# Kernel tuning notes

Hardware: AMD Instinct MI355X
Metric: run time of the kernel (lower is better)

Reference implementation:

```python
import jax, jax.numpy as jnp
import numpy as np
import math

N, C, H, W = 4, 256, 64, 64
CH = C // 2  # theta/phi output channels


def setup_inputs() -> dict:
    key = jax.random.key(0)
    k1, k2, k3 = jax.random.split(key, 3)
    x = jax.random.normal(k1, (N, C, H, W), dtype=jnp.float32)
    # 1x1 conv weights, init normal(0, 0.01) as in reset_params
    theta_w = 0.01 * jax.random.normal(k2, (CH, C), dtype=jnp.float32)
    phi_w = 0.01 * jax.random.normal(k3, (CH, C), dtype=jnp.float32)
    theta_b = jnp.zeros((CH,), dtype=jnp.float32)
    phi_b = jnp.zeros((CH,), dtype=jnp.float32)
    return {"x": x, "theta_w": theta_w, "theta_b": theta_b, "phi_w": phi_w, "phi_b": phi_b}


def reference(x, theta_w, theta_b, phi_w, phi_b):
    n, c, h, w = x.shape
    hw = h * w
    scale = 1.0 / math.sqrt(c)  # divide by sqrt(self.in_ch)
    # 1x1 convs (pointwise channel mixes)
    q = jnp.einsum('nchw,dc->ndhw', x, theta_w) + theta_b[None, :, None, None]
    k = jnp.einsum('nchw,dc->ndhw', x, phi_w) + phi_b[None, :, None, None]
    # affinity: [n, hw, hw] (flattened 'nabcd' tensor)
    q2 = q.reshape(n, c // 2, hw)
    k2 = k.reshape(n, c // 2, hw)
    ff = jnp.einsum('nis,nit->nst', q2, k2) * scale
    attn = jax.nn.softmax(ff, axis=-1)
    # weighted sum of values x: out[n,i,s] = sum_t attn[n,s,t] x[n,i,t]
    out = jnp.einsum('nst,nit->nis', attn, x.reshape(n, c, hw))
    return out.reshape(x.shape)
```

## Files before the change

### kernel.cpp

```cpp
#include <hip/hip_runtime.h>

#define S_LEN 4096
#define C_CH  256
#define D_CH  128
#define LAMBDA 0.09016844005555896f

typedef __attribute__((ext_vector_type(8)))  short short8;
typedef __attribute__((ext_vector_type(4)))  float f32x4;
typedef __attribute__((ext_vector_type(16))) float f32x16;

union PFrag { unsigned u[4]; short8 v; };

static __device__ __forceinline__ unsigned short f2bf(float x) {
    union { float f; unsigned u; } v; v.f = x;
    unsigned r = v.u + 0x7FFFu + ((v.u >> 16) & 1u);
    return (unsigned short)(r >> 16);
}

static __device__ __forceinline__ void gload_lds16(const void* g, void* l) {
    __builtin_amdgcn_global_load_lds(
        (const __attribute__((address_space(1))) void*)g,
        (__attribute__((address_space(3))) void*)l, 16, 0, 0);
}

__global__ void nlm_conv_kernel(const float* __restrict__ x, unsigned short* __restrict__ xb) {
    size_t base = ((size_t)blockIdx.x * 256 + threadIdx.x) * 4;
    float4 v = *reinterpret_cast<const float4*>(x + base);
    ushort4 b; b.x = f2bf(v.x); b.y = f2bf(v.y); b.z = f2bf(v.z); b.w = f2bf(v.w);
    *reinterpret_cast<ushort4*>(xb + base) = b;
}

__global__ void nlm_wconv_kernel(const float* __restrict__ tw, const float* __restrict__ pw,
                                 unsigned short* __restrict__ wb) {
    int base = (blockIdx.x * 256 + threadIdx.x) * 4;
    const float* src = (base < 32768) ? (tw + base) : (pw + base - 32768);
    float4 v = *reinterpret_cast<const float4*>(src);
    ushort4 b; b.x = f2bf(v.x); b.y = f2bf(v.y); b.z = f2bf(v.z); b.w = f2bf(v.w);
    *reinterpret_cast<ushort4*>(wb + base) = b;
}

__launch_bounds__(256, 1)
__global__ void nlm_proj_kernel(const float* __restrict__ x,
                                const unsigned short* __restrict__ wb,
                                const float* __restrict__ tb, const float* __restrict__ pbias,
                                unsigned char* __restrict__ Qb8, unsigned char* __restrict__ Kb8) {
    const int n    = blockIdx.y;
    const int wave = threadIdx.x >> 6;
    const int lane = threadIdx.x & 63;
    const int sl   = lane & 15, g = lane >> 4;
    const int s0   = blockIdx.x * 64 + wave * 16;
    const float* xn = x + (size_t)n * C_CH * S_LEN;

    f32x4 acc[16];
    #pragma unroll
    for (int i = 0; i < 16; ++i) acc[i] = (f32x4){0.f, 0.f, 0.f, 0.f};

    #pragma unroll 1
    for (int cc = 0; cc < 8; ++cc) {
        short8 af;
        #pragma unroll
        for (int j = 0; j < 8; ++j) {
            float v = xn[(size_t)(cc * 32 + g * 8 + j) * S_LEN + s0 + sl];
            af[j] = (short)f2bf(v);
        }
        #pragma unroll
        for (int t = 0; t < 16; ++t) {
            const unsigned short* wp = wb + (size_t)(t >> 3) * (D_CH * C_CH)
                                          + (size_t)((t & 7) * 16 + sl) * C_CH + cc * 32 + g * 8;
            short8 bf = *reinterpret_cast<const short8*>(wp);
            acc[t] = __builtin_amdgcn_mfma_f32_16x16x32_bf16(af, bf, acc[t], 0, 0, 0);
        }
    }
    #pragma unroll
    for (int t = 0; t < 16; ++t) {
        const float bias = (t < 8 ? tb : pbias)[(t & 7) * 16 + sl];
        unsigned char* dst = (t < 8 ? Qb8 : Kb8) + (size_t)n * S_LEN * D_CH;
        const int col = (t & 7) * 16 + sl;
        float v0 = acc[t][0] + bias, v1 = acc[t][1] + bias;
        float v2 = acc[t][2] + bias, v3 = acc[t][3] + bias;
        unsigned u01, u23;
        asm("v_cvt_pk_fp8_f32 %0, %1, %2" : "=v"(u01) : "v"(v0), "v"(v1));
        asm("v_cvt_pk_fp8_f32 %0, %1, %2" : "=v"(u23) : "v"(v2), "v"(v3));
        dst[(size_t)(s0 + g * 4 + 0) * D_CH + col] = (unsigned char)(u01 & 0xff);
        dst[(size_t)(s0 + g * 4 + 1) * D_CH + col] = (unsigned char)((u01 >> 8) & 0xff);
        dst[(size_t)(s0 + g * 4 + 2) * D_CH + col] = (unsigned char)(u23 & 0xff);
        dst[(size_t)(s0 + g * 4 + 3) * D_CH + col] = (unsigned char)((u23 >> 8) & 0xff);
    }
}

template<int TSPLIT>
__launch_bounds__(512, 2)
__global__ void nlm_attn_kernel(const unsigned char* __restrict__ Qb8,
                                const unsigned char* __restrict__ Kb8,
                                const unsigned short* __restrict__ xb,
                                float* __restrict__ part0, float* __restrict__ part1,
                                float* __restrict__ part2, float* __restrict__ part3,
                                float* __restrict__ lbuf) {
    constexpr int TRANGE = S_LEN / TSPLIT;
    constexpr int NITv   = TRANGE / 64;
    constexpr int TOTAL  = 64 * TSPLIT;
    const int sid  = blockIdx.x;
    const int newb = (sid & 7) * (TOTAL / 8) + (sid >> 3);
    const int n    = newb / (16 * TSPLIT);
    const int th   = (newb >> 4) & (TSPLIT - 1);
    const int sb   = newb & 15;
    const int lane = threadIdx.x & 63;
    const int wave = threadIdx.x >> 6;
    const int l31  = lane & 31;
    const int h    = lane >> 5;
    const int s0   = sb * 256 + wave * 32;
    const int tbase = th * TRANGE;

    __shared__ unsigned char  Klds[2][64 * 128];
    __shared__ unsigned short Vlds[2][256 * 64];

    const unsigned char* Qn8 = Qb8 + (size_t)n * S_LEN * D_CH;
    const unsigned char* Kn8 = Kb8 + (size_t)n * S_LEN * D_CH;
    const unsigned short* xn = xb + (size_t)n * C_CH * S_LEN;

    long qf8[8];
    #pragma unroll
    for (int ks = 0; ks < 8; ++ks)
        qf8[ks] = *reinterpret_cast<const long*>(Qn8 + (size_t)(s0 + l31) * D_CH + ks * 16 + h * 8);

    f32x16 oacc[8];
    #pragma unroll
    for (int i = 0; i < 8; ++i)
        #pragma unroll
        for (int r = 0; r < 16; ++r) oacc[i][r] = 0.f;
    float lsum = 0.f;

    auto kstage = [&](int itv, int slot) {
        const int it = itv < NITv ? itv : NITv - 1;
        const int t0 = tbase + it * 64;
        const int rl = wave * 8 + (lane >> 3);
        const int ch = (lane & 7) ^ (rl & 7);
        gload_lds16(Kn8 + (size_t)(t0 + rl) * D_CH + ch * 16,
                    &Klds[slot][wave * 8 * 128]);
    };
    auto vstage = [&](int itv, int slot) {
        const int it = itv < NITv ? itv : NITv - 1;
        const int t0 = tbase + it * 64;
        #pragma unroll
        for (int i = 0; i < 4; ++i) {
            const int row = wave * 32 + i * 8 + (lane >> 3);
            const int ch = (lane & 7) ^ (row & 7);
            gload_lds16(xn + (size_t)row * S_LEN + t0 + ch * 8,
                        &Vlds[slot][(wave * 32 + i * 8) * 64]);
        }
    };

    kstage(0, 0); vstage(0, 0);
    asm volatile("s_waitcnt vmcnt(0)" ::: "memory");

    #pragma unroll 1
    for (int it = 0; it < NITv; ++it) {
        const int cur = it & 1;
        __builtin_amdgcn_s_barrier();
        __builtin_amdgcn_sched_barrier(0);
        kstage(it + 1, cur ^ 1);
        vstage(it + 1, cur ^ 1);

        f32x16 sa, sb2;
        #pragma unroll
        for (int r = 0; r < 16; ++r) { sa[r] = 0.f; sb2[r] = 0.f; }
        const int f = l31 & 7;
        __builtin_amdgcn_s_setprio(1);
        #pragma unroll
        for (int ks = 0; ks < 8; ++ks) {
            const int co = ((ks ^ f) * 16) + h * 8;
            long kflo = *reinterpret_cast<const long*>(&Klds[cur][l31 * 128 + co]);
            long kfhi = *reinterpret_cast<const long*>(&Klds[cur][(32 + l31) * 128 + co]);
            sa  = __builtin_amdgcn_mfma_f32_32x32x16_fp8_fp8(kflo, qf8[ks], sa,  0, 0, 0);
            sb2 = __builtin_amdgcn_mfma_f32_32x32x16_fp8_fp8(kfhi, qf8[ks], sb2, 0, 0, 0);
        }
        __builtin_amdgcn_s_setprio(0);

        PFrag pa0, pa1, pa2, pa3;
        float rs = 0.f;
        {
            float p[16];
            #pragma unroll
            for (int r = 0; r < 16; ++r) { p[r] = __builtin_amdgcn_exp2f(sa[r] * LAMBDA); rs += p[r]; }
            unsigned W0, W1, W2, W3, W4, W5, W6, W7;
            asm("v_cvt_pk_bf16_f32 %0, %1, %2" : "=v"(W0) : "v"(p[0]),  "v"(p[1]));
            asm("v_cvt_pk_bf16_f32 %0, %1, %2" : "=v"(W1) : "v"(p[2]),  "v"(p[3]));
            asm("v_cvt_pk_bf16_f32 %0, %1, %2" : "=v"(W2) : "v"(p[4]),  "v"(p[5]));
            asm("v_cvt_pk_bf16_f32 %0, %1, %2" : "=v"(W3) : "v"(p[6]),  "v"(p[7]));
            asm("v_cvt_pk_bf16_f32 %0, %1, %2" : "=v"(W4) : "v"(p[8]),  "v"(p[9]));
            asm("v_cvt_pk_bf16_f32 %0, %1, %2" : "=v"(W5) : "v"(p[10]), "v"(p[11]));
            asm("v_cvt_pk_bf16_f32 %0, %1, %2" : "=v"(W6) : "v"(p[12]), "v"(p[13]));
            asm("v_cvt_pk_bf16_f32 %0, %1, %2" : "=v"(W7) : "v"(p[14]), "v"(p[15]));
            asm("v_permlane32_swap_b32 %0, %1" : "+v"(W0), "+v"(W2));
            asm("v_permlane32_swap_b32 %0, %1" : "+v"(W1), "+v"(W3));
            asm("v_permlane32_swap_b32 %0, %1" : "+v"(W4), "+v"(W6));
            asm("v_permlane32_swap_b32 %0, %1" : "+v"(W5), "+v"(W7));
            pa0.u[0] = W0; pa0.u[1] = W1; pa0.u[2] = W2; pa0.u[3] = W3;
            pa1.u[0] = W4; pa1.u[1] = W5; pa1.u[2] = W6; pa1.u[3] = W7;
        }
        {
            float p[16];
            #pragma unroll
            for (int r = 0; r < 16; ++r) { p[r] = __builtin_amdgcn_exp2f(sb2[r] * LAMBDA); rs += p[r]; }
            unsigned W0, W1, W2, W3, W4, W5, W6, W7;
            asm("v_cvt_pk_bf16_f32 %0, %1, %2" : "=v"(W0) : "v"(p[0]),  "v"(p[1]));
            asm("v_cvt_pk_bf16_f32 %0, %1, %2" : "=v"(W1) : "v"(p[2]),  "v"(p[3]));
            asm("v_cvt_pk_bf16_f32 %0, %1, %2" : "=v"(W2) : "v"(p[4]),  "v"(p[5]));
            asm("v_cvt_pk_bf16_f32 %0, %1, %2" : "=v"(W3) : "v"(p[6]),  "v"(p[7]));
            asm("v_cvt_pk_bf16_f32 %0, %1, %2" : "=v"(W4) : "v"(p[8]),  "v"(p[9]));
            asm("v_cvt_pk_bf16_f32 %0, %1, %2" : "=v"(W5) : "v"(p[10]), "v"(p[11]));
            asm("v_cvt_pk_bf16_f32 %0, %1, %2" : "=v"(W6) : "v"(p[12]), "v"(p[13]));
            asm("v_cvt_pk_bf16_f32 %0, %1, %2" : "=v"(W7) : "v"(p[14]), "v"(p[15]));
            asm("v_permlane32_swap_b32 %0, %1" : "+v"(W0), "+v"(W2));
            asm("v_permlane32_swap_b32 %0, %1" : "+v"(W1), "+v"(W3));
            asm("v_permlane32_swap_b32 %0, %1" : "+v"(W4), "+v"(W6));
            asm("v_permlane32_swap_b32 %0, %1" : "+v"(W5), "+v"(W7));
            pa2.u[0] = W0; pa2.u[1] = W1; pa2.u[2] = W2; pa2.u[3] = W3;
            pa3.u[0] = W4; pa3.u[1] = W5; pa3.u[2] = W6; pa3.u[3] = W7;
        }
        lsum += rs;

        __builtin_amdgcn_s_setprio(1);
        #pragma unroll
        for (int cb = 0; cb < 8; ++cb) {
            const int c = cb * 32 + l31;
            const unsigned short* Vr = &Vlds[cur][c * 64];
            const int fv = l31 & 7;
            short8 vf0 = *reinterpret_cast<const short8*>(&Vr[((0 + h) ^ fv) * 8]);
            short8 vf1 = *reinterpret_cast<const short8*>(&Vr[((2 + h) ^ fv) * 8]);
            short8 vf2 = *reinterpret_cast<const short8*>(&Vr[((4 + h) ^ fv) * 8]);
            short8 vf3 = *reinterpret_cast<const short8*>(&Vr[((6 + h) ^ fv) * 8]);
            oacc[cb] = __builtin_amdgcn_mfma_f32_32x32x16_bf16(vf0, pa0.v, oacc[cb], 0, 0, 0);
            oacc[cb] = __builtin_amdgcn_mfma_f32_32x32x16_bf16(vf1, pa1.v, oacc[cb], 0, 0, 0);
            oacc[cb] = __builtin_amdgcn_mfma_f32_32x32x16_bf16(vf2, pa2.v, oacc[cb], 0, 0, 0);
            oacc[cb] = __builtin_amdgcn_mfma_f32_32x32x16_bf16(vf3, pa3.v, oacc[cb], 0, 0, 0);
        }
        __builtin_amdgcn_s_setprio(0);

        asm volatile("s_waitcnt vmcnt(0)" ::: "memory");
        __builtin_amdgcn_sched_barrier(0);
    }

    float lt = lsum + __shfl_xor(lsum, 32);
    float* dst = (th == 0) ? part0 : (th == 1) ? part1 : (th == 2) ? part2 : part3;
    if (lane < 32) lbuf[th * 16384 + n * 4096 + s0 + lane] = lt;
    float* on = dst + (size_t)n * C_CH * S_LEN;
    #pragma unroll
    for (int cb = 0; cb < 8; ++cb) {
        #pragma unroll
        for (int r = 0; r < 16; ++r) {
            const int c = cb * 32 + (r & 3) + 8 * (r >> 2) + 4 * h;
            on[(size_t)c * S_LEN + s0 + l31] = oacc[cb][r];
        }
    }
}

template<int TSPLIT>
__global__ void nlm_combine_kernel(float* __restrict__ out, const float* __restrict__ p1,
                                   const float* __restrict__ p2, const float* __restrict__ p3,
                                   const float* __restrict__ lbuf) {
    const size_t e0 = ((size_t)blockIdx.x * 256 + threadIdx.x) * 4;
    const int n = (int)(e0 >> 20);
    const int s = (int)(e0 & 4095);
    float4 o = *reinterpret_cast<const float4*>(out + e0);
    float4 l = *reinterpret_cast<const float4*>(lbuf + n * 4096 + s);
    {
        float4 ov = *reinterpret_cast<const float4*>(p1 + e0);
        float4 lv = *reinterpret_cast<const float4*>(lbuf + 16384 + n * 4096 + s);
        o.x += ov.x; o.y += ov.y; o.z += ov.z; o.w += ov.w;
        l.x += lv.x; l.y += lv.y; l.z += lv.z; l.w += lv.w;
    }
    if (TSPLIT == 4) {
        float4 ov = *reinterpret_cast<const float4*>(p2 + e0);
        float4 lv = *reinterpret_cast<const float4*>(lbuf + 2 * 16384 + n * 4096 + s);
        o.x += ov.x; o.y += ov.y; o.z += ov.z; o.w += ov.w;
        l.x += lv.x; l.y += lv.y; l.z += lv.z; l.w += lv.w;
        float4 ow = *reinterpret_cast<const float4*>(p3 + e0);
        float4 lw = *reinterpret_cast<const float4*>(lbuf + 3 * 16384 + n * 4096 + s);
        o.x += ow.x; o.y += ow.y; o.z += ow.z; o.w += ow.w;
        l.x += lw.x; l.y += lw.y; l.z += lw.z; l.w += lw.w;
    }
    float4 r;
    r.x = o.x / l.x; r.y = o.y / l.y; r.z = o.z / l.z; r.w = o.w / l.w;
    *reinterpret_cast<float4*>(out + e0) = r;
}

extern "C" void kernel_launch(void* const* d_in, const int* in_sizes, int n_in,
                              void* d_out, int out_size, void* d_ws, size_t ws_size,
                              hipStream_t stream) {
    const float* x  = (const float*)d_in[0];
    const float* tw = (const float*)d_in[1];
    const float* tb = (const float*)d_in[2];
    const float* pw = (const float*)d_in[3];
    const float* pb = (const float*)d_in[4];
    float* out = (float*)d_out;

    char* ws = (char*)d_ws;
    unsigned short* xb = (unsigned short*)(ws);
    unsigned char*  Qb8 = (unsigned char*)(ws + 8388608);
    unsigned char*  Kb8 = (unsigned char*)(ws + 12582912);
    unsigned short* wb = (unsigned short*)(ws + 16777216);
    float*          lb = (float*)(ws + 16908288);
    float*          p1 = (float*)(ws + 17825792);
    float*          p2 = (float*)(ws + 34603008);
    float*          p3 = (float*)(ws + 51380224);

    nlm_conv_kernel<<<4096, 256, 0, stream>>>(x, xb);
    nlm_wconv_kernel<<<64, 256, 0, stream>>>(tw, pw, wb);
    nlm_proj_kernel<<<dim3(64, 4), 256, 0, stream>>>(x, wb, tb, pb, Qb8, Kb8);
    if (ws_size >= (size_t)68157440) {
        nlm_attn_kernel<4><<<256, 512, 0, stream>>>(Qb8, Kb8, xb, out, p1, p2, p3, lb);
        nlm_combine_kernel<4><<<4096, 256, 0, stream>>>(out, p1, p2, p3, lb);
    } else {
        nlm_attn_kernel<2><<<128, 512, 0, stream>>>(Qb8, Kb8, xb, out, p1, p1, p1, lb);
        nlm_combine_kernel<2><<<4096, 256, 0, stream>>>(out, p1, p1, p1, lb);
    }
}
```

Measured before the change: 98.55 us.

## Fuse split-K combine into attention kernel via last-block atomic counter

Removes the separate combine kernel. Each attention block bumps an atomic counter for its (n, s-block) group, and the last of the four T-split blocks to arrive sums the partials, normalizes by the summed softmax denominators and writes the output. It also remaps block indices so th is the outermost index. This saves a kernel launch and its tail, but the final reduction is serialized inside the last-arriving blocks. It also adds a memset and drops the fallback path for smaller workspaces.

Result: slower. 121.0 us (+22.8%).

```diff
diff --git a/kernel.cpp b/kernel.cpp
--- a/kernel.cpp
+++ b/kernel.cpp
@@ -88,22 +88,20 @@
     }
 }
 
-template<int TSPLIT>
 __launch_bounds__(512, 2)
 __global__ void nlm_attn_kernel(const unsigned char* __restrict__ Qb8,
                                 const unsigned char* __restrict__ Kb8,
                                 const unsigned short* __restrict__ xb,
                                 float* __restrict__ part0, float* __restrict__ part1,
                                 float* __restrict__ part2, float* __restrict__ part3,
-                                float* __restrict__ lbuf) {
-    constexpr int TRANGE = S_LEN / TSPLIT;
+                                float* __restrict__ lbuf, int* __restrict__ cnt) {
+    constexpr int TRANGE = S_LEN / 4;
     constexpr int NITv   = TRANGE / 64;
-    constexpr int TOTAL  = 64 * TSPLIT;
     const int sid  = blockIdx.x;
-    const int newb = (sid & 7) * (TOTAL / 8) + (sid >> 3);
-    const int n    = newb / (16 * TSPLIT);
-    const int th   = (newb >> 4) & (TSPLIT - 1);
-    const int sb   = newb & 15;
+    const int gidx = (sid & 7) * 8 + ((sid >> 3) & 7);
+    const int th   = sid >> 6;
+    const int n    = gidx >> 4;
+    const int sb   = gidx & 15;
     const int lane = threadIdx.x & 63;
     const int wave = threadIdx.x >> 6;
     const int l31  = lane & 31;
@@ -113,6 +111,7 @@
 
     __shared__ unsigned char  Klds[2][64 * 128];
     __shared__ unsigned short Vlds[2][256 * 64];
+    __shared__ int lastflag;
 
     const unsigned char* Qn8 = Qb8 + (size_t)n * S_LEN * D_CH;
     const unsigned char* Kn8 = Kb8 + (size_t)n * S_LEN * D_CH;
@@ -253,36 +252,31 @@
             on[(size_t)c * S_LEN + s0 + l31] = oacc[cb][r];
         }
     }
-}
-
-template<int TSPLIT>
-__global__ void nlm_combine_kernel(float* __restrict__ out, const float* __restrict__ p1,
-                                   const float* __restrict__ p2, const float* __restrict__ p3,
-                                   const float* __restrict__ lbuf) {
-    const size_t e0 = ((size_t)blockIdx.x * 256 + threadIdx.x) * 4;
-    const int n = (int)(e0 >> 20);
-    const int s = (int)(e0 & 4095);
-    float4 o = *reinterpret_cast<const float4*>(out + e0);
-    float4 l = *reinterpret_cast<const float4*>(lbuf + n * 4096 + s);
-    {
-        float4 ov = *reinterpret_cast<const float4*>(p1 + e0);
-        float4 lv = *reinterpret_cast<const float4*>(lbuf + 16384 + n * 4096 + s);
-        o.x += ov.x; o.y += ov.y; o.z += ov.z; o.w += ov.w;
-        l.x += lv.x; l.y += lv.y; l.z += lv.z; l.w += lv.w;
-    }
-    if (TSPLIT == 4) {
-        float4 ov = *reinterpret_cast<const float4*>(p2 + e0);
-        float4 lv = *reinterpret_cast<const float4*>(lbuf + 2 * 16384 + n * 4096 + s);
-        o.x += ov.x; o.y += ov.y; o.z += ov.z; o.w += ov.w;
-        l.x += lv.x; l.y += lv.y; l.z += lv.z; l.w += lv.w;
-        float4 ow = *reinterpret_cast<const float4*>(p3 + e0);
-        float4 lw = *reinterpret_cast<const float4*>(lbuf + 3 * 16384 + n * 4096 + s);
-        o.x += ow.x; o.y += ow.y; o.z += ow.z; o.w += ow.w;
-        l.x += lw.x; l.y += lw.y; l.z += lw.z; l.w += lw.w;
-    }
-    float4 r;
-    r.x = o.x / l.x; r.y = o.y / l.y; r.z = o.z / l.z; r.w = o.w / l.w;
-    *reinterpret_cast<float4*>(out + e0) = r;
+
+    __syncthreads();
+    if (threadIdx.x == 0) {
+        __threadfence();
+        int old = atomicAdd(&cnt[gidx], 1);
+        lastflag = (old == 3);
+        __threadfence();
+    }
+    __syncthreads();
+    if (lastflag) {
+        const size_t nbase = (size_t)n * C_CH * S_LEN;
+        const int sidx = n * 4096 + s0 + l31;
+        const float li = 1.0f / (lbuf[sidx] + lbuf[16384 + sidx]
+                               + lbuf[2 * 16384 + sidx] + lbuf[3 * 16384 + sidx]);
+        #pragma unroll
+        for (int cb = 0; cb < 8; ++cb) {
+            #pragma unroll
+            for (int r = 0; r < 16; ++r) {
+                const int c = cb * 32 + (r & 3) + 8 * (r >> 2) + 4 * h;
+                const size_t idx = nbase + (size_t)c * S_LEN + s0 + l31;
+                float v = ((part0[idx] + part1[idx]) + part2[idx]) + part3[idx];
+                part0[idx] = v * li;
+            }
+        }
+    }
 }
 
 extern "C" void kernel_launch(void* const* d_in, const int* in_sizes, int n_in,
@@ -301,18 +295,14 @@
     unsigned char*  Kb8 = (unsigned char*)(ws + 12582912);
     unsigned short* wb = (unsigned short*)(ws + 16777216);
     float*          lb = (float*)(ws + 16908288);
+    int*            ct = (int*)(ws + 17170432);
     float*          p1 = (float*)(ws + 17825792);
     float*          p2 = (float*)(ws + 34603008);
     float*          p3 = (float*)(ws + 51380224);
 
+    hipMemsetAsync(ct, 0, 256, stream);
     nlm_conv_kernel<<<4096, 256, 0, stream>>>(x, xb);
     nlm_wconv_kernel<<<64, 256, 0, stream>>>(tw, pw, wb);
     nlm_proj_kernel<<<dim3(64, 4), 256, 0, stream>>>(x, wb, tb, pb, Qb8, Kb8);
-    if (ws_size >= (size_t)68157440) {
-        nlm_attn_kernel<4><<<256, 512, 0, stream>>>(Qb8, Kb8, xb, out, p1, p2, p3, lb);
-        nlm_combine_kernel<4><<<4096, 256, 0, stream>>>(out, p1, p2, p3, lb);
-    } else {
-        nlm_attn_kernel<2><<<128, 512, 0, stream>>>(Qb8, Kb8, xb, out, p1, p1, p1, lb);
-        nlm_combine_kernel<2><<<4096, 256, 0, stream>>>(out, p1, p1, p1, lb);
-    }
-}
+    nlm_attn_kernel<<<256, 512, 0, stream>>>(Qb8, Kb8, xb, out, p1, p2, p3, lb, ct);
+}
```
